# Kernel tuning notes

Hardware: AMD Instinct MI355X
Metric: run time of the kernel (lower is better)

The kernel has to match this reference:

```python
import jax, jax.numpy as jnp
import numpy as np
import math

D_MODEL = 2048
N_HEADS = 16
D_HEAD = D_MODEL // N_HEADS
MAX_T = 2048
B, T = 2, 2048


def rotate_half(x):
    # interleaved rotate: (x0,x1,x2,x3,...) -> (-x1,x0,-x3,x2,...)
    x1 = x[..., ::2]
    x2 = x[..., 1::2]
    return jnp.stack((-x2, x1), axis=-1).reshape(x.shape)


def setup_inputs() -> dict:
    key = jax.random.key(0)
    k1, k2, k3 = jax.random.split(key, 3)
    x = jax.random.normal(k1, (B, T, D_MODEL), dtype=jnp.float32)
    # torch nn.Linear weights: [out, in]
    s = 1.0 / math.sqrt(D_MODEL)
    Wqkv = jax.random.uniform(k2, (3 * D_MODEL, D_MODEL), dtype=jnp.float32, minval=-s, maxval=s)
    WO = jax.random.uniform(k3, (D_MODEL, D_MODEL), dtype=jnp.float32, minval=-s, maxval=s)
    return {"x": x, "Wqkv": Wqkv, "WO": WO}


def reference(x, Wqkv, WO):
    Bx, Tx, _ = x.shape
    # RoPE tables (buffers)
    pos = jnp.arange(Tx, dtype=jnp.float32)
    freqs = jnp.exp(-math.log(10000.0) * jnp.arange(0, D_HEAD, 2, dtype=jnp.float32) / D_HEAD)
    angles = pos[:, None] * freqs[None, :]               # [T, d_head/2]
    sin = jnp.repeat(jnp.sin(angles), 2, axis=-1)        # [T, d_head]
    cos = jnp.repeat(jnp.cos(angles), 2, axis=-1)
    sin = sin[None, None, :, :]
    cos = cos[None, None, :, :]

    qkv = x @ Wqkv.T                                     # [B, T, 3D]
    q, k, v = jnp.split(qkv, 3, axis=-1)
    def to_heads(t):
        return t.reshape(Bx, Tx, N_HEADS, D_HEAD).transpose(0, 2, 1, 3)  # [B,H,T,d]
    q, k, v = to_heads(q), to_heads(k), to_heads(v)

    q = q * cos + rotate_half(q) * sin
    k = k * cos + rotate_half(k) * sin

    scores = jnp.einsum('bhqd,bhkd->bhqk', q, k) / math.sqrt(D_HEAD)
    mask = jnp.triu(jnp.full((Tx, Tx), -jnp.inf, dtype=scores.dtype), k=1)
    scores = scores + mask
    attn = jax.nn.softmax(scores, axis=-1)
    out = jnp.einsum('bhqk,bhkd->bhqd', attn, v)
    out = out.transpose(0, 2, 1, 3).reshape(Bx, Tx, D_MODEL)
    return out @ WO.T
```

## Files before the change

kernel.cpp:

```cpp
#include <hip/hip_runtime.h>
#include <hip/hip_bf16.h>

typedef unsigned short u16;
typedef __attribute__((ext_vector_type(8))) short bf16x8;
typedef __attribute__((ext_vector_type(4))) float f32x4;

#define B_   2
#define T_   2048
#define DM   2048
#define NH   16
#define DH   128
#define NQKV 6144

__device__ __forceinline__ u16 f2bf(float f) {
  __hip_bfloat16 h = __float2bfloat16(f);
  u16 u; __builtin_memcpy(&u, &h, 2); return u;
}
__device__ __forceinline__ float bf2f(u16 u) {
  __hip_bfloat16 h; __builtin_memcpy(&h, &u, 2); return __bfloat162float(h);
}
__device__ __forceinline__ void gl_lds16(const void* g, void* l) {
  __builtin_amdgcn_global_load_lds(
      (__attribute__((address_space(1))) unsigned int*)g,
      (__attribute__((address_space(3))) unsigned int*)l, 16, 0, 0);
}
__device__ __forceinline__ f32x4 MFMA(bf16x8 a, bf16x8 b, f32x4 c) {
  return __builtin_amdgcn_mfma_f32_16x16x32_bf16(a, b, c, 0, 0, 0);
}

__global__ __launch_bounds__(256) void cast_kernel(const float* __restrict__ in,
                                                   u16* __restrict__ out, int n4) {
  int i = blockIdx.x * 256 + threadIdx.x;
  if (i >= n4) return;
  float4 v = ((const float4*)in)[i];
  ushort4 o;
  o.x = f2bf(v.x); o.y = f2bf(v.y); o.z = f2bf(v.z); o.w = f2bf(v.w);
  ((ushort4*)out)[i] = o;
}

__global__ __launch_bounds__(256) void rope_tab(float2* __restrict__ tab) {
  int idx = blockIdx.x * 256 + threadIdx.x;
  if (idx >= T_ * 64) return;
  int t = idx >> 6, i = idx & 63;
  float freq = __expf(-9.210340371976184f * (float)i / 64.0f);
  float sn, cs;
  sincosf((float)t * freq, &sn, &cs);
  tab[idx] = make_float2(cs, sn);
}

#define G1_M 4096
#define G1_N 6144
#define G1_K 2048

#define MFMA_Q(AQ, M0)                                                        \
  _Pragma("unroll") for (int e_ = 0; e_ < 2; ++e_)                            \
  _Pragma("unroll") for (int n_ = 0; n_ < 4; ++n_)                            \
  _Pragma("unroll") for (int kb_ = 0; kb_ < 2; ++kb_)                         \
    acc[(M0) + e_][n_] = MFMA(AQ[e_][kb_], bfr[n_][kb_], acc[(M0) + e_][n_])

#define BARRIER() asm volatile("s_barrier" ::: "memory")
#define LGKM0()                                                               \
  do {                                                                        \
    asm volatile("s_waitcnt lgkmcnt(0)" ::: "memory");                        \
    __builtin_amdgcn_sched_barrier(0);                                        \
  } while (0)
#define SBAR() __builtin_amdgcn_sched_barrier(0)

__global__ __launch_bounds__(512, 2) void gemm1_8ph(const u16* __restrict__ A,
                                                    const u16* __restrict__ Bm,
                                                    const float2* __restrict__ tab,
                                                    u16* __restrict__ Qo,
                                                    u16* __restrict__ Ko,
                                                    u16* __restrict__ Vt) {
  __shared__ alignas(16) u16 As[2][256 * 64];
  __shared__ alignas(16) u16 Bs[2][256 * 64];
  const int tid = threadIdx.x;
  const int w = tid >> 6, lane = tid & 63;
  const int lrow = lane & 15, quad = lane >> 4;
  const long tileM = (long)blockIdx.y * 256, tileN = (long)blockIdx.x * 256;
  const int wm = (w >> 2) * 128, wn = (w & 3) * 64;

  const int sw8 = w * 8;
  const int srowL = lane >> 3;
  const int schunk = ((lane & 7) ^ srowL) * 8;
  const u16* Ag0 = A + (tileM + sw8 + srowL) * (long)G1_K + schunk;
  const u16* Bg0 = Bm + (tileN + sw8 + srowL) * (long)G1_K + schunk;

  auto stgA = [&](int tt, int h) {
    const int b = tt & 1;
    gl_lds16(Ag0 + (size_t)(h * 128) * G1_K + tt * 64,
             &As[b][(h * 128 + sw8) * 64]);
    gl_lds16(Ag0 + (size_t)(h * 128 + 64) * G1_K + tt * 64,
             &As[b][(h * 128 + 64 + sw8) * 64]);
  };
  auto stgB = [&](int tt, int h) {
    const int b = tt & 1;
    gl_lds16(Bg0 + (size_t)(h * 128) * G1_K + tt * 64,
             &Bs[b][(h * 128 + sw8) * 64]);
    gl_lds16(Bg0 + (size_t)(h * 128 + 64) * G1_K + tt * 64,
             &Bs[b][(h * 128 + 64 + sw8) * 64]);
  };

  const int aBase = (wm + lrow) * 64;
  const int bBase = (wn + lrow) * 64;
  const int slot[2] = { (quad ^ (lrow & 7)) * 8, ((4 + quad) ^ (lrow & 7)) * 8 };

  f32x4 acc[8][4] = {};
  bf16x8 bfr[4][2];
  bf16x8 aCur[2][2], aNxt[2][2];

  stgA(0, 0); stgA(0, 1); stgB(0, 0); stgB(0, 1);
  stgB(1, 0); stgB(1, 1); stgA(1, 0);
  asm volatile("s_waitcnt vmcnt(6)" ::: "memory");
  BARRIER();
#pragma unroll
  for (int ni = 0; ni < 4; ++ni)
#pragma unroll
    for (int kb = 0; kb < 2; ++kb)
      bfr[ni][kb] = *(const bf16x8*)(Bs[0] + bBase + ni * 1024 + slot[kb]);
#pragma unroll
  for (int e = 0; e < 2; ++e)
#pragma unroll
    for (int kb = 0; kb < 2; ++kb)
      aCur[e][kb] = *(const bf16x8*)(As[0] + aBase + e * 1024 + slot[kb]);

#pragma unroll 1
  for (int t = 0; t < 32; ++t) {
    const u16* AsC = As[t & 1];
    LGKM0();
    __builtin_amdgcn_s_setprio(1);
    MFMA_Q(aCur, 0);
    __builtin_amdgcn_s_setprio(0);
    SBAR();
#pragma unroll
    for (int e = 0; e < 2; ++e)
#pragma unroll
      for (int kb = 0; kb < 2; ++kb)
        aNxt[e][kb] = *(const bf16x8*)(AsC + aBase + (2 + e) * 1024 + slot[kb]);
    if (t + 1 < 32) stgA(t + 1, 1);
    BARRIER();
    LGKM0();
    __builtin_amdgcn_s_setprio(1);
    MFMA_Q(aNxt, 2);
    __builtin_amdgcn_s_setprio(0);
    SBAR();
#pragma unroll
    for (int e = 0; e < 2; ++e)
#pragma unroll
      for (int kb = 0; kb < 2; ++kb)
        aCur[e][kb] = *(const bf16x8*)(AsC + aBase + (4 + e) * 1024 + slot[kb]);
    if (t + 2 < 32) stgB(t + 2, 0);
    BARRIER();
    LGKM0();
    __builtin_amdgcn_s_setprio(1);
    MFMA_Q(aCur, 4);
    __builtin_amdgcn_s_setprio(0);
    SBAR();
#pragma unroll
    for (int e = 0; e < 2; ++e)
#pragma unroll
      for (int kb = 0; kb < 2; ++kb)
        aNxt[e][kb] = *(const bf16x8*)(AsC + aBase + (6 + e) * 1024 + slot[kb]);
    if (t + 2 < 32) stgB(t + 2, 1);
    if (t < 30) { asm volatile("s_waitcnt vmcnt(4)" ::: "memory"); }
    else       { asm volatile("s_waitcnt vmcnt(0)" ::: "memory"); }
    BARRIER();
    LGKM0();
    __builtin_amdgcn_s_setprio(1);
    MFMA_Q(aNxt, 6);
    __builtin_amdgcn_s_setprio(0);
    SBAR();
    if (t + 1 < 32) {
      const u16* AsN = As[(t + 1) & 1];
      const u16* BsN = Bs[(t + 1) & 1];
#pragma unroll
      for (int ni = 0; ni < 4; ++ni)
#pragma unroll
        for (int kb = 0; kb < 2; ++kb)
          bfr[ni][kb] = *(const bf16x8*)(BsN + bBase + ni * 1024 + slot[kb]);
#pragma unroll
      for (int e = 0; e < 2; ++e)
#pragma unroll
        for (int kb = 0; kb < 2; ++kb)
          aCur[e][kb] = *(const bf16x8*)(AsN + aBase + e * 1024 + slot[kb]);
    }
    if (t + 2 < 32) stgA(t + 2, 0);
    BARRIER();
  }

  const long crow = tileM + wm + quad * 4;
  const long ccol = tileN + wn + lrow;
  const int sec = (int)(tileN >> 11);
  const int bI = (int)(tileM >> 11);
  const int tG0 = (int)(tileM & 2047);
  if (sec < 2) {
    u16* dst = sec == 0 ? Qo : Ko;
    const float scale = sec == 0 ? 0.08838834764831845f : 1.0f;
#pragma unroll
    for (int ni = 0; ni < 4; ++ni) {
      const int col = (int)((ccol + ni * 16) & 2047);
      const int h = col >> 7, d = col & 127;
      const int i = d >> 1;
      const float2* tcol = tab + i;
#pragma unroll
      for (int mi = 0; mi < 8; ++mi) {
        const int rowL = wm + mi * 16 + quad * 4;
#pragma unroll
        for (int r = 0; r < 4; ++r) {
          const int tt = tG0 + rowL + r;
          float x = acc[mi][ni][r];
          float p = __shfl_xor(x, 1);
          float2 sc = tcol[(size_t)tt * 64];
          float o = (x * sc.x + ((d & 1) ? p : -p) * sc.y) * scale;
          dst[(((size_t)(bI * 16 + h)) * T_ + tt) * DH + d] = f2bf(o);
        }
      }
    }
  } else {
#pragma unroll
    for (int ni = 0; ni < 4; ++ni) {
      const int col = (int)((ccol + ni * 16) & 2047);
      const int h = col >> 7, d = col & 127;
#pragma unroll
      for (int mi = 0; mi < 8; ++mi) {
        const int t0 = tG0 + wm + mi * 16 + quad * 4;
        ushort4 v4;
        v4.x = f2bf(acc[mi][ni][0]);
        v4.y = f2bf(acc[mi][ni][1]);
        v4.z = f2bf(acc[mi][ni][2]);
        v4.w = f2bf(acc[mi][ni][3]);
        *(ushort4*)(Vt + (((size_t)(bI * 16 + h)) * DH + d) * (size_t)T_ + t0) = v4;
      }
    }
  }
}

__global__ __launch_bounds__(256) void gemm_bt(const u16* __restrict__ A,
                                               const u16* __restrict__ Bm,
                                               void* __restrict__ Cp,
                                               int M, int N, int K, int out_f32) {
  __shared__ u16 As[128 * 64];
  __shared__ u16 Bs[128 * 64];
  const int tid  = threadIdx.x;
  const int wave = tid >> 6, lane = tid & 63;
  const int lrow = lane & 15, quad = lane >> 4;
  const long tileM = (long)blockIdx.y * 128, tileN = (long)blockIdx.x * 128;
  const int wm = (wave >> 1) * 64, wn = (wave & 1) * 64;
  const int sRowIn = lane >> 3;
  const int sChunk = (lane & 7) ^ sRowIn;
  const int sRow0  = wave * 32 + sRowIn;
  const u16* Ag = A + (tileM + sRow0) * (long)K + sChunk * 8;
  const u16* Bg = Bm + (tileN + sRow0) * (long)K + sChunk * 8;
  u16* AsW = As + wave * 2048;
  u16* BsW = Bs + wave * 2048;
  f32x4 acc[4][4] = {};
  for (int kt = 0; kt < K; kt += 64) {
#pragma unroll
    for (int i = 0; i < 4; ++i)
      gl_lds16(Ag + kt + (size_t)i * 8 * K, AsW + i * 512);
#pragma unroll
    for (int i = 0; i < 4; ++i)
      gl_lds16(Bg + kt + (size_t)i * 8 * K, BsW + i * 512);
    __syncthreads();
#pragma unroll
    for (int kb = 0; kb < 2; ++kb) {
      const int slot8 = (((kb * 4 + quad) ^ (lrow & 7)) * 8);
      bf16x8 af[4], bfr[4];
#pragma unroll
      for (int i = 0; i < 4; ++i)
        af[i]  = *(const bf16x8*)(As + (wm + i * 16 + lrow) * 64 + slot8);
#pragma unroll
      for (int i = 0; i < 4; ++i)
        bfr[i] = *(const bf16x8*)(Bs + (wn + i * 16 + lrow) * 64 + slot8);
#pragma unroll
      for (int mi = 0; mi < 4; ++mi)
#pragma unroll
        for (int ni = 0; ni < 4; ++ni)
          acc[mi][ni] = MFMA(af[mi], bfr[ni], acc[mi][ni]);
    }
    __syncthreads();
  }
  const long crow = tileM + wm + quad * 4;
  const long ccol = tileN + wn + lrow;
  if (out_f32) {
    float* C = (float*)Cp;
#pragma unroll
    for (int mi = 0; mi < 4; ++mi)
#pragma unroll
      for (int ni = 0; ni < 4; ++ni)
#pragma unroll
        for (int r = 0; r < 4; ++r)
          C[(crow + mi * 16 + r) * (long)N + (ccol + ni * 16)] = acc[mi][ni][r];
  } else {
    u16* C = (u16*)Cp;
#pragma unroll
    for (int mi = 0; mi < 4; ++mi)
#pragma unroll
      for (int ni = 0; ni < 4; ++ni)
#pragma unroll
        for (int r = 0; r < 4; ++r)
          C[(crow + mi * 16 + r) * (long)N + (ccol + ni * 16)] = f2bf(acc[mi][ni][r]);
  }
}

__global__ __launch_bounds__(512) void attn_flash(const u16* __restrict__ Q,
                                                  const u16* __restrict__ K,
                                                  const u16* __restrict__ Vt,
                                                  u16* __restrict__ AO) {
  __shared__ u16 Kl[64 * 128];
  __shared__ u16 Vl[128 * 64];
  __shared__ u16 Pl[8 * 16 * 64];
  const int pairIdx = blockIdx.x;
  const int bh = blockIdx.y;
  const int b = bh >> 4, h = bh & 15;
  const int tid = threadIdx.x;
  const int wave = tid >> 6, lane = tid & 63;
  const int lrow = lane & 15, quad = lane >> 4;
  const u16* Qb = Q + (size_t)bh * T_ * DH;
  const u16* Kb = K + (size_t)bh * T_ * DH;
  const u16* Vb = Vt + (size_t)bh * DH * T_;

  u16* KlW = Kl + wave * 1024;
  u16* VlW = Vl + wave * 1024;
  const int kRowIn = lane >> 4;
  const int vRowIn = lane >> 3;
  const int vChunk = (lane & 7) ^ vRowIn;
  u16* PlW = Pl + wave * 1024;

  for (int pass = 0; pass < 2; ++pass) {
    const int qt = pass == 0 ? (15 - pairIdx) : pairIdx;
    const int qbase = qt * 128;
    const int nkt = 2 * qt + 2;

    bf16x8 qf[4];
    {
      const u16* qrow = Qb + (size_t)(qbase + wave * 16 + lrow) * DH + quad * 8;
#pragma unroll
      for (int kc = 0; kc < 4; ++kc) qf[kc] = *(const bf16x8*)(qrow + kc * 32);
    }
    f32x4 o[8] = {};
    float lsum[4] = {0.f, 0.f, 0.f, 0.f};

    for (int j = 0; j < nkt; ++j) {
#pragma unroll
      for (int i = 0; i < 2; ++i) {
        int krow = wave * 8 + i * 4 + kRowIn;
        int kch = (lane & 15) ^ (krow & 15);
        gl_lds16(Kb + (size_t)(j * 64 + krow) * DH + kch * 8, KlW + i * 512);
      }
#pragma unroll
      for (int i = 0; i < 2; ++i) {
        int vd = wave * 16 + i * 8 + vRowIn;
        gl_lds16(Vb + (size_t)vd * T_ + j * 64 + vChunk * 8, VlW + i * 512);
      }
      __syncthreads();

      f32x4 s[4] = {};
#pragma unroll
      for (int kc = 0; kc < 4; ++kc)
#pragma unroll
        for (int ns = 0; ns < 4; ++ns) {
          bf16x8 kf = *(const bf16x8*)(Kl + (ns * 16 + lrow) * 128 +
                                       (((kc * 4 + quad) ^ lrow) * 8));
          s[ns] = MFMA(qf[kc], kf, s[ns]);
        }
      if (j >= 2 * qt) {
        const int jl = (j - 2 * qt) * 64;
#pragma unroll
        for (int ns = 0; ns < 4; ++ns)
#pragma unroll
          for (int r = 0; r < 4; ++r)
            if (jl + ns * 16 + lrow > wave * 16 + quad * 4 + r)
              s[ns][r] = -__builtin_inff();
      }
#pragma unroll
      for (int r = 0; r < 4; ++r) {
        const int prow = quad * 4 + r;
#pragma unroll
        for (int ns = 0; ns < 4; ++ns) {
          float p = __expf(s[ns][r]);
          PlW[prow * 64 + (((ns * 2 + (lrow >> 3)) ^ (prow & 7)) * 8) +
              (lrow & 7)] = f2bf(p);
          lsum[r] += p;
        }
      }

#pragma unroll
      for (int kc = 0; kc < 2; ++kc) {
        bf16x8 pf = *(const bf16x8*)(PlW + lrow * 64 +
                                     (((kc * 4 + quad) ^ (lrow & 7)) * 8));
#pragma unroll
        for (int os = 0; os < 8; ++os) {
          bf16x8 vf = *(const bf16x8*)(Vl + (os * 16 + lrow) * 64 +
                                       (((kc * 4 + quad) ^ (lrow & 7)) * 8));
          o[os] = MFMA(pf, vf, o[os]);
        }
      }
      __syncthreads();
    }
#pragma unroll
    for (int r = 0; r < 4; ++r) {
      lsum[r] += __shfl_xor(lsum[r], 1, 16);
      lsum[r] += __shfl_xor(lsum[r], 2, 16);
      lsum[r] += __shfl_xor(lsum[r], 4, 16);
      lsum[r] += __shfl_xor(lsum[r], 8, 16);
    }
#pragma unroll
    for (int r = 0; r < 4; ++r) {
      float inv = 1.0f / lsum[r];
      const size_t row = (size_t)b * T_ + qbase + wave * 16 + quad * 4 + r;
      u16* dst = AO + row * DM + h * DH;
#pragma unroll
      for (int os = 0; os < 8; ++os) dst[os * 16 + lrow] = f2bf(o[os][r] * inv);
    }
  }
}

extern "C" void kernel_launch(void* const* d_in, const int* in_sizes, int n_in,
                              void* d_out, int out_size, void* d_ws, size_t ws_size,
                              hipStream_t stream) {
  const float* x    = (const float*)d_in[0];
  const float* Wqkv = (const float*)d_in[1];
  const float* WO   = (const float*)d_in[2];
  char* ws = (char*)d_ws;
  size_t off = 0;
  u16* xb   = (u16*)(ws + off); off += (size_t)B_ * T_ * DM * 2;
  u16* wqb  = (u16*)(ws + off); off += (size_t)NQKV * DM * 2;
  u16* wob  = (u16*)(ws + off); off += (size_t)DM * DM * 2;
  u16* Qb   = (u16*)(ws + off); off += (size_t)B_ * NH * T_ * DH * 2;
  u16* Kb   = (u16*)(ws + off); off += (size_t)B_ * NH * T_ * DH * 2;
  u16* Vtb  = (u16*)(ws + off); off += (size_t)B_ * NH * T_ * DH * 2;
  float2* tabp = (float2*)(ws + off); off += (size_t)T_ * 64 * 8;
  u16* AO   = xb;

  rope_tab<<<(T_ * 64 + 255) / 256, 256, 0, stream>>>(tabp);
  cast_kernel<<<(B_ * T_ * DM / 4 + 255) / 256, 256, 0, stream>>>(x, xb, B_ * T_ * DM / 4);
  cast_kernel<<<(NQKV * DM / 4 + 255) / 256, 256, 0, stream>>>(Wqkv, wqb, NQKV * DM / 4);
  cast_kernel<<<(DM * DM / 4 + 255) / 256, 256, 0, stream>>>(WO, wob, DM * DM / 4);

  gemm1_8ph<<<dim3(G1_N / 256, G1_M / 256), 512, 0, stream>>>(xb, wqb, tabp,
                                                              Qb, Kb, Vtb);

  attn_flash<<<dim3(8, B_ * NH), 512, 0, stream>>>(Qb, Kb, Vtb, AO);

  gemm_bt<<<dim3(DM / 128, B_ * T_ / 128), 256, 0, stream>>>(
      AO, wob, d_out, B_ * T_, DM, DM, 1);
}
```

Before: 369.9 us.

## Double-buffer K/V tiles in flash attention to overlap loads with compute

Measured after the change: 370.1 us. No clear change (+0.0%).

```diff
diff --git a/kernel.cpp b/kernel.cpp
--- a/kernel.cpp
+++ b/kernel.cpp
@@ -307,8 +307,8 @@
                                                   const u16* __restrict__ K,
                                                   const u16* __restrict__ Vt,
                                                   u16* __restrict__ AO) {
-  __shared__ u16 Kl[64 * 128];
-  __shared__ u16 Vl[128 * 64];
+  __shared__ u16 Kl[2][64 * 128];
+  __shared__ u16 Vl[2][128 * 64];
   __shared__ u16 Pl[8 * 16 * 64];
   const int pairIdx = blockIdx.x;
   const int bh = blockIdx.y;
@@ -320,13 +320,27 @@
   const u16* Kb = K + (size_t)bh * T_ * DH;
   const u16* Vb = Vt + (size_t)bh * DH * T_;
 
-  u16* KlW = Kl + wave * 1024;
-  u16* VlW = Vl + wave * 1024;
   const int kRowIn = lane >> 4;
   const int vRowIn = lane >> 3;
   const int vChunk = (lane & 7) ^ vRowIn;
   u16* PlW = Pl + wave * 1024;
 
+  auto stageKV = [&](int j, int buf) {
+#pragma unroll
+    for (int i = 0; i < 2; ++i) {
+      int krow = wave * 8 + i * 4 + kRowIn;
+      int kch = (lane & 15) ^ (krow & 15);
+      gl_lds16(Kb + (size_t)(j * 64 + krow) * DH + kch * 8,
+               Kl[buf] + wave * 1024 + i * 512);
+    }
+#pragma unroll
+    for (int i = 0; i < 2; ++i) {
+      int vd = wave * 16 + i * 8 + vRowIn;
+      gl_lds16(Vb + (size_t)vd * T_ + j * 64 + vChunk * 8,
+               Vl[buf] + wave * 1024 + i * 512);
+    }
+  };
+
   for (int pass = 0; pass < 2; ++pass) {
     const int qt = pass == 0 ? (15 - pairIdx) : pairIdx;
     const int qbase = qt * 128;
@@ -341,26 +355,26 @@
     f32x4 o[8] = {};
     float lsum[4] = {0.f, 0.f, 0.f, 0.f};
 
+    stageKV(0, 0);
+
     for (int j = 0; j < nkt; ++j) {
-#pragma unroll
-      for (int i = 0; i < 2; ++i) {
-        int krow = wave * 8 + i * 4 + kRowIn;
-        int kch = (lane & 15) ^ (krow & 15);
-        gl_lds16(Kb + (size_t)(j * 64 + krow) * DH + kch * 8, KlW + i * 512);
-      }
-#pragma unroll
-      for (int i = 0; i < 2; ++i) {
-        int vd = wave * 16 + i * 8 + vRowIn;
-        gl_lds16(Vb + (size_t)vd * T_ + j * 64 + vChunk * 8, VlW + i * 512);
-      }
-      __syncthreads();
-
+      const int cb = j & 1;
+      if (j + 1 < nkt) {
+        stageKV(j + 1, cb ^ 1);
+        asm volatile("s_waitcnt vmcnt(4)" ::: "memory");
+      } else {
+        asm volatile("s_waitcnt vmcnt(0)" ::: "memory");
+      }
+      BARRIER();
+
+      const u16* KlC = Kl[cb];
+      const u16* VlC = Vl[cb];
       f32x4 s[4] = {};
 #pragma unroll
       for (int kc = 0; kc < 4; ++kc)
 #pragma unroll
         for (int ns = 0; ns < 4; ++ns) {
-          bf16x8 kf = *(const bf16x8*)(Kl + (ns * 16 + lrow) * 128 +
+          bf16x8 kf = *(const bf16x8*)(KlC + (ns * 16 + lrow) * 128 +
                                        (((kc * 4 + quad) ^ lrow) * 8));
           s[ns] = MFMA(qf[kc], kf, s[ns]);
         }
@@ -391,12 +405,13 @@
                                      (((kc * 4 + quad) ^ (lrow & 7)) * 8));
 #pragma unroll
         for (int os = 0; os < 8; ++os) {
-          bf16x8 vf = *(const bf16x8*)(Vl + (os * 16 + lrow) * 64 +
+          bf16x8 vf = *(const bf16x8*)(VlC + (os * 16 + lrow) * 64 +
                                        (((kc * 4 + quad) ^ (lrow & 7)) * 8));
           o[os] = MFMA(pf, vf, o[os]);
         }
       }
-      __syncthreads();
+      asm volatile("s_waitcnt lgkmcnt(0)" ::: "memory");
+      BARRIER();
     }
 #pragma unroll
     for (int r = 0; r < 4; ++r) {
```
